# Kernel optimization log

Hardware: AMD Instinct MI355X
Metric: run time of the kernel (lower is better)

## Reference

```python
import jax, jax.numpy as jnp
import numpy as np

M = 1536   # rows (users)
N = 1536   # cols (items)
P_ROW = 4  # Chebyshev order over rows
P_COL = 4  # Chebyshev order over cols
OUT = 32   # out_channels_GCCN


def cheb_basis(L, order):
    """Stack of Chebyshev polynomials T_k(L), shape (order+1, n, n)."""
    n = L.shape[0]
    Ts = [jnp.eye(n, dtype=L.dtype)]
    if order > 0:
        Ts.append(L)
    for _ in range(2, order + 1):
        Ts.append(2.0 * (L @ Ts[-1]) - Ts[-2])
    return jnp.stack(Ts)


def setup_inputs() -> dict:
    key = jax.random.key(0)
    kx, kr, kc, kt = jax.random.split(key, 4)
    x = jax.random.normal(kx, (1, M, N), dtype=jnp.float32)
    # Scaled symmetric 'Laplacians' with spectral radius < 1 so the
    # Chebyshev recursion stays numerically stable.
    Ar = jax.random.normal(kr, (M, M), dtype=jnp.float32)
    Lr = (Ar + Ar.T) / (4.0 * jnp.sqrt(jnp.float32(M)))
    Ac = jax.random.normal(kc, (N, N), dtype=jnp.float32)
    Lc = (Ac + Ac.T) / (4.0 * jnp.sqrt(jnp.float32(N)))
    theta = jax.random.normal(kt, (P_ROW + 1, P_COL + 1, 1, OUT), dtype=jnp.float32) * 0.05
    bias = jnp.zeros((OUT,), dtype=jnp.float32)
    return {"x": x, "Lr": Lr, "Lc": Lc, "theta": theta, "bias": bias}


def reference(x, Lr, Lc, theta, bias):
    # Chebyshev bases: Tr (p_row+1, M, M), Tc (p_col+1, N, N)
    Tr = cheb_basis(Lr, theta.shape[0] - 1)
    Tc = cheb_basis(Lc, theta.shape[1] - 1)
    # Stage 1: row transform -> (i, c, M, N)
    x_row = jnp.einsum('imp,cpn->icmn', Tr, x)
    # Stage 2: col transform -> (i, j, c, M, N)
    basis_feats = jnp.einsum('icmn,jnk->ijcmk', x_row, Tc)
    # Stage 3: bilinear weights -> (OUT, M, N)
    out = jnp.einsum('ijcmn,ijco->omn', basis_feats, theta)
    return out + bias[:, None, None]
```

## Files before the change

kernel.cpp:

```cpp
#include <hip/hip_runtime.h>
#include <hip/hip_bf16.h>


#define NDIM 1536
#define PM (NDIM * NDIM)

typedef __attribute__((ext_vector_type(8))) short bf16x8;
typedef __attribute__((ext_vector_type(4))) float f32x4;

__device__ inline void gload_lds16(const void* g, void* l) {
  __builtin_amdgcn_global_load_lds(
      (const __attribute__((address_space(1))) void*)g,
      (__attribute__((address_space(3))) void*)l, 16, 0, 0);
}

__device__ inline unsigned short f2bf(float f) {
  __hip_bfloat16 h = __float2bfloat16(f);
  return *reinterpret_cast<unsigned short*>(&h);
}
__device__ inline float bf2f(unsigned short u) {
  return __uint_as_float((unsigned)u << 16);
}

struct ZSet {
  const unsigned short* A;
  const unsigned short* Bt;
  unsigned short* out;
  const unsigned short* Cp;
  int mode;
};
struct ZSet4 { ZSet z[4]; };

__global__ __launch_bounds__(256) void gemm_k(ZSet4 zs) {
  const ZSet zp = zs.z[blockIdx.z];
  __shared__ __align__(16) unsigned short As[128 * 32];
  __shared__ __align__(16) unsigned short Bs[128 * 32];
  const int tid = threadIdx.x;
  const int lane = tid & 63;
  const int wave = tid >> 6;
  const int wm = wave >> 1, wn = wave & 1;
  const int gm0 = blockIdx.y * 128;
  const int jn = blockIdx.x / 12;
  const int nloc0 = (blockIdx.x % 12) * 128;
  const int q = lane >> 4;
  const int rowl = lane & 15;

  const unsigned short* Btb = zp.Bt + (size_t)jn * PM;
  unsigned short* outb = zp.out + (size_t)jn * 5 * PM;

  f32x4 acc[4][4] = {};

  for (int k0 = 0; k0 < NDIM; k0 += 32) {
#pragma unroll
    for (int l = 0; l < 2; ++l) {
      int f = l * 256 + wave * 64 + lane;
      int r = f >> 2, kc = f & 3;
      const unsigned short* ga = zp.A + (size_t)(gm0 + r) * NDIM + k0 + kc * 8;
      const unsigned short* gb = Btb + (size_t)(nloc0 + r) * NDIM + k0 + kc * 8;
      unsigned short* la = &As[(size_t)(l * 256 + wave * 64) * 8];
      unsigned short* lb = &Bs[(size_t)(l * 256 + wave * 64) * 8];
      gload_lds16(ga, la);
      gload_lds16(gb, lb);
    }
    __syncthreads();
    bf16x8 af[4], bfv[4];
#pragma unroll
    for (int t = 0; t < 4; ++t) {
      af[t] = *(const bf16x8*)&As[(wm * 64 + t * 16 + rowl) * 32 + q * 8];
      bfv[t] = *(const bf16x8*)&Bs[(wn * 64 + t * 16 + rowl) * 32 + q * 8];
    }
#pragma unroll
    for (int mt = 0; mt < 4; ++mt)
#pragma unroll
      for (int nt = 0; nt < 4; ++nt)
        acc[mt][nt] = __builtin_amdgcn_mfma_f32_16x16x32_bf16(
            af[mt], bfv[nt], acc[mt][nt], 0, 0, 0);
    __syncthreads();
  }

#pragma unroll
  for (int mt = 0; mt < 4; ++mt) {
#pragma unroll
    for (int nt = 0; nt < 4; ++nt) {
#pragma unroll
      for (int v = 0; v < 4; ++v) {
        int row = gm0 + wm * 64 + mt * 16 + q * 4 + v;
        int col = nloc0 + wn * 64 + nt * 16 + rowl;
        size_t idx = (size_t)row * NDIM + col;
        float val = acc[mt][nt][v];
        if (zp.mode == 1) val = 2.0f * val - bf2f(zp.Cp[idx]);
        if (zp.mode == 2) val = 2.0f * val - (row == col ? 1.0f : 0.0f);
        outb[idx] = f2bf(val);
      }
    }
  }
}

__global__ void transpose_f2b(const float* __restrict__ in,
                              unsigned short* __restrict__ out16) {
  __shared__ float tile[32][33];
  int bx = blockIdx.x, by = blockIdx.y;
  int tx = threadIdx.x;
#pragma unroll
  for (int r = threadIdx.y; r < 32; r += 8)
    tile[r][tx] = in[(size_t)(by * 32 + r) * NDIM + bx * 32 + tx];
  __syncthreads();
  int ox = by * 32 + tx;
#pragma unroll
  for (int r = threadIdx.y; r < 32; r += 8)
    out16[(size_t)(bx * 32 + r) * NDIM + ox] = f2bf(tile[tx][r]);
}

__global__ void cast_bf16_k(const float* __restrict__ in,
                            unsigned short* __restrict__ out) {
  int i = (blockIdx.x * 256 + threadIdx.x) * 4;
  float4 v = *(const float4*)(in + i);
  ushort4 r;
  r.x = f2bf(v.x); r.y = f2bf(v.y); r.z = f2bf(v.z); r.w = f2bf(v.w);
  *(ushort4*)(out + i) = r;
}

__global__ __launch_bounds__(256, 2) void combine_k(
    const unsigned short* __restrict__ Z,
    const float* __restrict__ theta,
    const float* __restrict__ bias,
    float* __restrict__ out) {
  const size_t p0 = (size_t)(blockIdx.x * 256 + threadIdx.x) * 2;
  float z0[25], z1[25];
#pragma unroll
  for (int c = 0; c < 25; ++c) {
    unsigned int u = *(const unsigned int*)(Z + (size_t)c * PM + p0);
    z0[c] = __uint_as_float(u << 16);
    z1[c] = __uint_as_float(u & 0xffff0000u);
  }
  for (int o = 0; o < 32; ++o) {
    float b = bias[o];
    float a0 = b, a1 = b;
#pragma unroll
    for (int j = 0; j < 5; ++j)
#pragma unroll
      for (int i = 0; i < 5; ++i) {
        float t = theta[i * 160 + j * 32 + o];
        int c = j * 5 + i;
        a0 += t * z0[c];
        a1 += t * z1[c];
      }
    float2 w; w.x = a0; w.y = a1;
    *(float2*)(out + (size_t)o * PM + p0) = w;
  }
}

extern "C" void kernel_launch(void* const* d_in, const int* in_sizes, int n_in,
                              void* d_out, int out_size, void* d_ws, size_t ws_size,
                              hipStream_t stream) {
  (void)in_sizes; (void)n_in; (void)out_size; (void)ws_size;
  const float* X = (const float*)d_in[0];
  const float* Lr = (const float*)d_in[1];
  const float* Lc = (const float*)d_in[2];
  const float* theta = (const float*)d_in[3];
  const float* bias = (const float*)d_in[4];
  float* out = (float*)d_out;

  unsigned short* Zall = (unsigned short*)d_ws;
  unsigned short* Tr = Zall + (size_t)25 * PM;
  unsigned short* Tc = Tr + (size_t)4 * PM;
  unsigned short* Xt = Tc + (size_t)4 * PM;

  unsigned short* Tr0 = Tr;                 unsigned short* Tc0 = Tc;
  unsigned short* Tr1 = Tr + (size_t)PM;    unsigned short* Tc1 = Tc + (size_t)PM;
  unsigned short* Tr2 = Tr + (size_t)2*PM;  unsigned short* Tc2 = Tc + (size_t)2*PM;
  unsigned short* Tr3 = Tr + (size_t)3*PM;  unsigned short* Tc3 = Tc + (size_t)3*PM;

  cast_bf16_k<<<PM / 1024, 256, 0, stream>>>(Lr, Tr0);
  cast_bf16_k<<<PM / 1024, 256, 0, stream>>>(Lc, Tc0);
  cast_bf16_k<<<PM / 1024, 256, 0, stream>>>(X, Zall);
  transpose_f2b<<<dim3(48, 48), dim3(32, 8), 0, stream>>>(X, Xt);

  {
    ZSet4 a{};
    a.z[0] = {Tr0, Tr0, Tr1, nullptr, 2};
    a.z[1] = {Tc0, Tc0, Tc1, nullptr, 2};
    gemm_k<<<dim3(12, 12, 2), 256, 0, stream>>>(a);
  }
  {
    ZSet4 a{};
    a.z[0] = {Tr0, Tr1, Tr2, Tr0, 1};
    a.z[1] = {Tr1, Tr1, Tr3, nullptr, 2};
    a.z[2] = {Tc0, Tc1, Tc2, Tc0, 1};
    a.z[3] = {Tc1, Tc1, Tc3, nullptr, 2};
    gemm_k<<<dim3(12, 12, 4), 256, 0, stream>>>(a);
  }
  {
    ZSet4 a{};
    a.z[0] = {Tr, Xt, Zall + (size_t)PM, nullptr, 0};
    gemm_k<<<dim3(12, 48, 1), 256, 0, stream>>>(a);
  }
  {
    ZSet4 a{};
    a.z[0] = {Zall, Tc0, Zall + (size_t)5 * PM, nullptr, 0};
    gemm_k<<<dim3(48, 60, 1), 256, 0, stream>>>(a);
  }

  combine_k<<<PM / 512, 256, 0, stream>>>(Zall, theta, bias, out);
}
```

Baseline: 783.5 us.

## Add 256x256 double-buffered swizzled GEMM kernel for the large basis GEMMs

Adds a new GEMM kernel that uses 256x256 tiles with 8 waves, a k-tile of 64, and double-buffered LDS with an XOR swizzle. The kernel splits each k-tile into four MFMA phases, interleaving async global-to-LDS loads with compute, and uses barriers and s_setprio to schedule them. The two large stage GEMMs (row and column transforms) now use this kernel, while the small Chebyshev GEMMs keep the old one. The aim is more data reuse per tile, fewer LDS bank conflicts, and load latency hidden behind MFMA work. The cost is higher register and LDS pressure, plus fewer, larger blocks.

```diff
diff --git a/kernel.cpp b/kernel.cpp
--- a/kernel.cpp
+++ b/kernel.cpp
@@ -4,6 +4,7 @@
 
 #define NDIM 1536
 #define PM (NDIM * NDIM)
+#define NK 24
 
 typedef __attribute__((ext_vector_type(8))) short bf16x8;
 typedef __attribute__((ext_vector_type(4))) float f32x4;
@@ -30,6 +31,163 @@
   int mode;
 };
 struct ZSet4 { ZSet z[4]; };
+
+#define PH_MID()                                       \
+  do {                                                 \
+    asm volatile("" ::: "memory");                     \
+    __builtin_amdgcn_s_barrier();                      \
+    asm volatile("s_waitcnt lgkmcnt(0)" ::: "memory"); \
+    __builtin_amdgcn_sched_barrier(0);                 \
+    __builtin_amdgcn_s_setprio(1);                     \
+  } while (0)
+
+#define PH_END()                                       \
+  do {                                                 \
+    __builtin_amdgcn_s_setprio(0);                     \
+    asm volatile("" ::: "memory");                     \
+    __builtin_amdgcn_s_barrier();                      \
+  } while (0)
+
+__global__ __launch_bounds__(512, 2) void gemm256_k(ZSet4 zs) {
+  const ZSet zp = zs.z[blockIdx.z];
+  __shared__ __align__(16) unsigned short As[2][2][8192];
+  __shared__ __align__(16) unsigned short Bs[2][2][8192];
+  const int tid = threadIdx.x;
+  const int lane = tid & 63;
+  const int wave = tid >> 6;
+  const int wm = wave >> 2, wn = wave & 3;
+  const int gm0 = blockIdx.y * 256;
+  const int jn = blockIdx.x / 6;
+  const int nloc0 = (blockIdx.x % 6) * 256;
+  const int q = lane >> 4;
+  const int rowl = lane & 15;
+  const unsigned short* Ab = zp.A;
+  const unsigned short* Btb = zp.Bt + (size_t)jn * PM;
+  unsigned short* outb = zp.out + (size_t)jn * 5 * PM;
+
+  bf16x8 a[4][2];
+  bf16x8 b0[2][2], b1[2][2];
+  f32x4 acc00[4][2] = {}, acc01[4][2] = {}, acc10[4][2] = {}, acc11[4][2] = {};
+
+  auto stageA = [&](int buf, int h, int kt) {
+#pragma unroll
+    for (int l = 0; l < 2; ++l) {
+      const int o = (wave * 2 + l) * 1024 + lane * 16;
+      const int wms = o >> 13;
+      const int r = (o >> 7) & 63;
+      const int s = (o >> 4) & 7;
+      const unsigned short* src =
+          Ab + (size_t)(gm0 + wms * 128 + h * 64 + r) * NDIM + kt * 64 +
+          ((s ^ (r & 7)) << 3);
+      gload_lds16(src, &As[buf][h][(wave * 2 + l) * 512]);
+    }
+  };
+  auto stageB = [&](int buf, int h, int kt) {
+#pragma unroll
+    for (int l = 0; l < 2; ++l) {
+      const int o = (wave * 2 + l) * 1024 + lane * 16;
+      const int wns = o >> 12;
+      const int r = (o >> 7) & 31;
+      const int s = (o >> 4) & 7;
+      const unsigned short* src =
+          Btb + (size_t)(nloc0 + wns * 64 + h * 32 + r) * NDIM + kt * 64 +
+          ((s ^ (r & 7)) << 3);
+      gload_lds16(src, &Bs[buf][h][(wave * 2 + l) * 512]);
+    }
+  };
+  auto loadA = [&](int buf, int h) {
+#pragma unroll
+    for (int mt = 0; mt < 4; ++mt) {
+      const int lr = mt * 16 + rowl;
+#pragma unroll
+      for (int ks = 0; ks < 2; ++ks) {
+        const int s0 = ks * 4 + q;
+        a[mt][ks] = *(const bf16x8*)&As[buf][h][wm * 4096 + lr * 64 +
+                                                ((s0 ^ (lr & 7)) << 3)];
+      }
+    }
+  };
+  auto loadB = [&](bf16x8 (&bb)[2][2], int buf, int h) {
+#pragma unroll
+    for (int nt = 0; nt < 2; ++nt) {
+      const int lr = nt * 16 + rowl;
+#pragma unroll
+      for (int ks = 0; ks < 2; ++ks) {
+        const int s0 = ks * 4 + q;
+        bb[nt][ks] = *(const bf16x8*)&Bs[buf][h][wn * 2048 + lr * 64 +
+                                                 ((s0 ^ (lr & 7)) << 3)];
+      }
+    }
+  };
+  auto mfma16 = [&](f32x4 (&ac)[4][2], bf16x8 (&bb)[2][2]) {
+#pragma unroll
+    for (int mt = 0; mt < 4; ++mt)
+#pragma unroll
+      for (int nt = 0; nt < 2; ++nt)
+#pragma unroll
+        for (int ks = 0; ks < 2; ++ks)
+          ac[mt][nt] = __builtin_amdgcn_mfma_f32_16x16x32_bf16(
+              a[mt][ks], bb[nt][ks], ac[mt][nt], 0, 0, 0);
+  };
+
+  stageA(0, 0, 0); stageB(0, 0, 0); stageB(0, 1, 0); stageA(0, 1, 0);
+  stageA(1, 0, 1); stageB(1, 0, 1); stageB(1, 1, 1);
+  asm volatile("s_waitcnt vmcnt(6)" ::: "memory");
+  __builtin_amdgcn_s_barrier();
+
+  auto ktile = [&](int kt, int b) {
+    loadA(b, 0);
+    loadB(b0, b, 0);
+    if (kt + 1 < NK) stageA(b ^ 1, 1, kt + 1);
+    PH_MID();
+    mfma16(acc00, b0);
+    PH_END();
+    loadB(b1, b, 1);
+    if (kt + 2 < NK) stageA(b, 0, kt + 2);
+    PH_MID();
+    mfma16(acc01, b1);
+    PH_END();
+    loadA(b, 1);
+    if (kt + 2 < NK) stageB(b, 0, kt + 2);
+    PH_MID();
+    mfma16(acc11, b1);
+    PH_END();
+    if (kt + 2 < NK) {
+      stageB(b, 1, kt + 2);
+      asm volatile("s_waitcnt vmcnt(6)" ::: "memory");
+    } else {
+      asm volatile("s_waitcnt vmcnt(0)" ::: "memory");
+    }
+    PH_MID();
+    mfma16(acc10, b0);
+    PH_END();
+  };
+  for (int kt = 0; kt < NK; kt += 2) {
+    ktile(kt, 0);
+    ktile(kt + 1, 1);
+  }
+
+  auto writeQ = [&](f32x4 (&ac)[4][2], int mh, int nh) {
+#pragma unroll
+    for (int mt = 0; mt < 4; ++mt)
+#pragma unroll
+      for (int nt = 0; nt < 2; ++nt)
+#pragma unroll
+        for (int v = 0; v < 4; ++v) {
+          const int row = gm0 + wm * 128 + mh * 64 + mt * 16 + q * 4 + v;
+          const int col = nloc0 + wn * 64 + nh * 32 + nt * 16 + rowl;
+          const size_t idx = (size_t)row * NDIM + col;
+          float val = ac[mt][nt][v];
+          if (zp.mode == 1) val = 2.0f * val - bf2f(zp.Cp[idx]);
+          if (zp.mode == 2) val = 2.0f * val - (row == col ? 1.0f : 0.0f);
+          outb[idx] = f2bf(val);
+        }
+  };
+  writeQ(acc00, 0, 0);
+  writeQ(acc01, 0, 1);
+  writeQ(acc11, 1, 1);
+  writeQ(acc10, 1, 0);
+}
 
 __global__ __launch_bounds__(256) void gemm_k(ZSet4 zs) {
   const ZSet zp = zs.z[blockIdx.z];
@@ -193,12 +351,12 @@
   {
     ZSet4 a{};
     a.z[0] = {Tr, Xt, Zall + (size_t)PM, nullptr, 0};
-    gemm_k<<<dim3(12, 48, 1), 256, 0, stream>>>(a);
+    gemm256_k<<<dim3(6, 24, 1), 512, 0, stream>>>(a);
   }
   {
     ZSet4 a{};
     a.z[0] = {Zall, Tc0, Zall + (size_t)5 * PM, nullptr, 0};
-    gemm_k<<<dim3(48, 60, 1), 256, 0, stream>>>(a);
+    gemm256_k<<<dim3(24, 30, 1), 512, 0, stream>>>(a);
   }
 
   combine_k<<<PM / 512, 256, 0, stream>>>(Zall, theta, bias, out);
```

Result: faster. 694.8 us (-11.3%).
